# Kernel tuning notes

Measured on AMD Instinct MI355X. Metric: run time of the kernel, lower is better.

## Reference

```python
import jax, jax.numpy as jnp
import numpy as np
import math

SIZE = 64
NLAND = 8
N_ITER = 6


def setup_inputs() -> dict:
    key = jax.random.key(0)
    k1, k2, k3 = jax.random.split(key, 3)
    B, T, C = 4, 4096, 1024
    return {
        "q": jax.random.normal(k1, (B, T, C), dtype=jnp.float32),
        "k": jax.random.normal(k2, (B, T, C), dtype=jnp.float32),
        "v": jax.random.normal(k3, (B, T, C), dtype=jnp.float32),
    }


def _iterative_pinv(mat, n_iter=N_ITER):
    # Newton-Schulz iteration for pseudo-inverse of [..., m, m] kernel.
    m = mat.shape[-1]
    I = jnp.eye(m, dtype=mat.dtype)
    K = mat
    # NOTE: torch.max over the whole tensor (global scalar), faithful to source.
    V = (1.0 / jnp.max(jnp.sum(K, axis=-2))) * jnp.swapaxes(K, -1, -2)
    for _ in range(n_iter):
        KV = jnp.matmul(K, V)
        V = jnp.matmul(0.25 * V, 13.0 * I - jnp.matmul(KV, 15.0 * I - jnp.matmul(KV, 7.0 * I - KV)))
    return V


def reference(q, k, v):
    B, T, C = q.shape
    H = C // SIZE
    scale = 1.0 / math.sqrt(SIZE)
    # Faithful reshape (not transpose) as in the source module.
    qh = q.reshape(B, H, T, SIZE)
    kh = k.reshape(B, H, T, SIZE)
    vh = v.reshape(B, H, T, SIZE)
    # T % NLAND == 0 branch: landmark = segment mean over T//NLAND tokens.
    q_l = qh.reshape(B, H, NLAND, T // NLAND, SIZE).mean(axis=-2)  # [B,H,m,d]
    k_l = kh.reshape(B, H, NLAND, T // NLAND, SIZE).mean(axis=-2)
    kernel_1 = jax.nn.softmax(jnp.einsum('bhtd,bhmd->bhtm', qh, k_l) * scale, axis=-1)  # [B,H,T,m]
    kernel_2 = jax.nn.softmax(jnp.einsum('bhmd,bhnd->bhmn', q_l, k_l) * scale, axis=-1)  # [B,H,m,m]
    kernel_3 = jax.nn.softmax(jnp.einsum('bhmd,bhtd->bhmt', q_l, kh) * scale, axis=-1)  # [B,H,m,T]
    pinv = _iterative_pinv(kernel_2)  # [B,H,m,m]
    k3v = jnp.matmul(kernel_3, vh)    # [B,H,m,d]
    out = jnp.matmul(jnp.matmul(kernel_1, pinv), k3v)  # [B,H,T,d]
    return out.reshape(B, T, C)
```

## Files before the change

kernel.cpp:

```cpp
#include <hip/hip_runtime.h>
#include <math.h>

#define T_TOK 4096
#define DD 64
#define NHEADS 64
#define SEG 512
#define SCALE 0.125f

#define QL_OFF   0
#define KL_OFF   32768
#define K2_OFF   65536
#define CS_OFF   69632
#define KP_OFF   70144
#define PA_OFF   332288
#define PD_OFF   2429440
#define W2_OFF   2462208
#define LPQ_OFF  2494976

#define WAVE_BAR() __builtin_amdgcn_wave_barrier()

__global__ __launch_bounds__(256) void qsum_kernel(
    const float* __restrict__ q, float* __restrict__ ws) {
  int tid = threadIdx.x;
  const float4* q4 = (const float4*)q + (size_t)blockIdx.x * 2048;
  float4 x[8];
#pragma unroll
  for (int i = 0; i < 8; ++i) x[i] = q4[i * 256 + tid];
  float4 a = make_float4(0.f, 0.f, 0.f, 0.f);
#pragma unroll
  for (int i = 0; i < 8; ++i) {
    a.x += x[i].x; a.y += x[i].y; a.z += x[i].z; a.w += x[i].w;
  }
  __shared__ float4 red[16][17];
  red[tid >> 4][tid & 15] = a;
  __syncthreads();
  if (tid < 16) {
    float4 s = make_float4(0.f, 0.f, 0.f, 0.f);
#pragma unroll
    for (int g = 0; g < 16; ++g) {
      float4 r = red[g][tid];
      s.x += r.x; s.y += r.y; s.z += r.z; s.w += r.w;
    }
    ((float4*)(ws + LPQ_OFF))[blockIdx.x * 16 + tid] = s;
  }
}

__global__ __launch_bounds__(512) void prepq_kernel(float* __restrict__ ws) {
  int hb = blockIdx.x, tid = threadIdx.x;
  int m = tid >> 6, d = tid & 63;
  float s = 0.f;
#pragma unroll
  for (int c2 = 0; c2 < 4; ++c2)
    s += ws[LPQ_OFF + (size_t)(hb * 32 + m * 4 + c2) * 64 + d];
  ws[QL_OFF + hb * 512 + tid] = s * (1.f / (float)SEG);
}

#define STAGE_AND_CONSUME(K0,K1,K2,K3,V0,V1,V2,V3)                            \
  {                                                                           \
    int r0_ = lane >> 4, c0_ = (lane & 15) * 4;                               \
    *(float4*)&kt[r0_][c0_] = K0;       *(float4*)&vt[r0_][c0_] = V0;         \
    *(float4*)&kt[r0_+4][c0_] = K1;     *(float4*)&vt[r0_+4][c0_] = V1;       \
    *(float4*)&kt[r0_+8][c0_] = K2;     *(float4*)&vt[r0_+8][c0_] = V2;       \
    *(float4*)&kt[r0_+12][c0_] = K3;    *(float4*)&vt[r0_+12][c0_] = V3;      \
    ks.x += K0.x+K1.x+K2.x+K3.x; ks.y += K0.y+K1.y+K2.y+K3.y;                 \
    ks.z += K0.z+K1.z+K2.z+K3.z; ks.w += K0.w+K1.w+K2.w+K3.w;                 \
  }                                                                           \
  WAVE_BAR();                                                                 \
  _Pragma("unroll")                                                           \
  for (int rep_ = 0; rep_ < 2; ++rep_) {                                      \
    int t_ = rep_ * 8 + (lane >> 3);                                          \
    const float4* kr_ = (const float4*)&kt[t_][0];                            \
    const float4* qr_ = (const float4*)&qls[m][0];                            \
    float dp_ = 0.f;                                                          \
    _Pragma("unroll")                                                         \
    for (int d4_ = 0; d4_ < 16; ++d4_) {                                      \
      float4 kv_ = kr_[d4_], qv_ = qr_[d4_];                                  \
      dp_ += kv_.x*qv_.x + kv_.y*qv_.y + kv_.z*qv_.z + kv_.w*qv_.w;           \
    }                                                                         \
    float p_ = __expf(dp_ * SCALE);                                           \
    pl[t_][m] = p_;                                                           \
    den += p_;                                                                \
  }                                                                           \
  WAVE_BAR();                                                                 \
  _Pragma("unroll")                                                           \
  for (int t_ = 0; t_ < 16; ++t_) {                                           \
    float4 vv_ = *(const float4*)&vt[t_][d4i * 4];                            \
    float pa_ = pl[t_][g];                                                    \
    float pb_ = pl[t_][g + 4];                                                \
    acc0.x += pa_*vv_.x; acc0.y += pa_*vv_.y; acc0.z += pa_*vv_.z; acc0.w += pa_*vv_.w; \
    acc1.x += pb_*vv_.x; acc1.y += pb_*vv_.y; acc1.z += pb_*vv_.z; acc1.w += pb_*vv_.w; \
  }                                                                           \
  WAVE_BAR();

__global__ __launch_bounds__(256) void kvpass_kernel(
    const float* __restrict__ k, const float* __restrict__ v,
    float* __restrict__ ws) {
  int tid = threadIdx.x;
  int w = tid >> 6, lane = tid & 63;
  int gw = blockIdx.x * 4 + w;
  int hb = gw >> 6;
  __shared__ float qls[8][68];
  __shared__ float kt_all[4][16][68];
  __shared__ float vt_all[4][16][68];
  __shared__ float pl_all[4][16][9];
  float (*kt)[68] = kt_all[w];
  float (*vt)[68] = vt_all[w];
  float (*pl)[9]  = pl_all[w];

  if (tid < 128) {
    float4 x = ((const float4*)(ws + QL_OFF))[hb * 128 + tid];
    *(float4*)&qls[tid >> 4][(tid & 15) * 4] = x;
  }
  __syncthreads();

  int m = lane & 7, g = lane >> 4, d4i = lane & 15;
  size_t tokbase = (size_t)gw * 64;
  const float4* k4 = (const float4*)k + tokbase * 16;
  const float4* v4 = (const float4*)v + tokbase * 16;

  float4 ks = make_float4(0.f, 0.f, 0.f, 0.f);
  float den = 0.f;
  float4 acc0 = make_float4(0.f, 0.f, 0.f, 0.f);
  float4 acc1 = make_float4(0.f, 0.f, 0.f, 0.f);

  float4 ka0 = k4[lane],       ka1 = k4[64 + lane],
         ka2 = k4[128 + lane], ka3 = k4[192 + lane];
  float4 va0 = v4[lane],       va1 = v4[64 + lane],
         va2 = v4[128 + lane], va3 = v4[192 + lane];

#pragma unroll 1
  for (int t2 = 0; t2 < 2; ++t2) {
    int bB = (t2 * 2 + 1) * 256;
    float4 kb0 = k4[bB + lane],       kb1 = k4[bB + 64 + lane],
           kb2 = k4[bB + 128 + lane], kb3 = k4[bB + 192 + lane];
    float4 vb0 = v4[bB + lane],       vb1 = v4[bB + 64 + lane],
           vb2 = v4[bB + 128 + lane], vb3 = v4[bB + 192 + lane];

    STAGE_AND_CONSUME(ka0, ka1, ka2, ka3, va0, va1, va2, va3)

    if (t2 == 0) {
      ka0 = k4[512 + lane];       ka1 = k4[512 + 64 + lane];
      ka2 = k4[512 + 128 + lane]; ka3 = k4[512 + 192 + lane];
      va0 = v4[512 + lane];       va1 = v4[512 + 64 + lane];
      va2 = v4[512 + 128 + lane]; va3 = v4[512 + 192 + lane];
    }

    STAGE_AND_CONSUME(kb0, kb1, kb2, kb3, vb0, vb1, vb2, vb3)
  }
  ks.x += __shfl_xor(ks.x, 16, 64); ks.y += __shfl_xor(ks.y, 16, 64);
  ks.z += __shfl_xor(ks.z, 16, 64); ks.w += __shfl_xor(ks.w, 16, 64);
  ks.x += __shfl_xor(ks.x, 32, 64); ks.y += __shfl_xor(ks.y, 32, 64);
  ks.z += __shfl_xor(ks.z, 32, 64); ks.w += __shfl_xor(ks.w, 32, 64);
  if (lane < 16)
    ((float4*)(ws + KP_OFF))[gw * 16 + lane] = ks;
  den += __shfl_xor(den, 8, 64);
  den += __shfl_xor(den, 16, 64);
  den += __shfl_xor(den, 32, 64);
  if (lane < 8)
    ws[PD_OFF + (size_t)gw * 8 + lane] = den;
  ((float4*)(ws + PA_OFF))[((size_t)gw * 8 + g) * 16 + d4i] = acc0;
  ((float4*)(ws + PA_OFF))[((size_t)gw * 8 + g + 4) * 16 + d4i] = acc1;
}

__global__ __launch_bounds__(512) void prepk_kernel(float* __restrict__ ws) {
  int hb = blockIdx.x, tid = threadIdx.x;
  __shared__ float qls[8][68];
  __shared__ float kls[8][68];
  __shared__ float ee[8][9];
  int m = tid >> 6, d = tid & 63;
  float s = 0.f;
#pragma unroll
  for (int j = 0; j < 8; ++j)
    s += ws[KP_OFF + (size_t)(hb * 64 + m * 8 + j) * 64 + d];
  s *= (1.f / (float)SEG);
  kls[m][d] = s;
  ws[KL_OFF + hb * 512 + tid] = s;
  qls[m][d] = ws[QL_OFF + hb * 512 + tid];
  __syncthreads();
  if (tid < 64) {
    int i = tid >> 3, j = tid & 7;
    float dot = 0.f;
#pragma unroll
    for (int dd = 0; dd < 64; ++dd) dot += qls[i][dd] * kls[j][dd];
    ee[i][j] = __expf(dot * SCALE);
  }
  __syncthreads();
  if (tid < 64) {
    int i = tid >> 3, j = tid & 7;
    float ssum = 0.f;
#pragma unroll
    for (int jj = 0; jj < 8; ++jj) ssum += ee[i][jj];
    ws[K2_OFF + hb * 64 + tid] = ee[i][j] / ssum;
  }
  if (tid < 8) {
    float cs = 0.f;
    for (int ii = 0; ii < 8; ++ii) {
      float ssum = 0.f;
#pragma unroll
      for (int jj = 0; jj < 8; ++jj) ssum += ee[ii][jj];
      cs += ee[ii][tid] / ssum;
    }
    ws[CS_OFF + hb * 8 + tid] = cs;
  }
}

__global__ __launch_bounds__(512) void pinvw2_kernel(float* __restrict__ ws) {
  int hb = blockIdx.x, tid = threadIdx.x;
  __shared__ float k3vs[8][68];
  __shared__ float K[8][9], V[8][9], X[8][9], Y[8][9];
  __shared__ float smax;
  int m = tid >> 6, d = tid & 63;
  float s = 0.f, den = 0.f;
  for (int c = 0; c < 64; ++c) {
    s += ws[PA_OFF + (((size_t)hb * 64 + c) * 8 + m) * 64 + d];
    den += ws[PD_OFF + ((size_t)hb * 64 + c) * 8 + m];
  }
  k3vs[m][d] = s / den;
  if (tid < 64) {
    float mx = 0.f;
    for (int t = 0; t < 8; ++t) mx = fmaxf(mx, ws[CS_OFF + t * 64 + tid]);
    for (int off = 32; off; off >>= 1) mx = fmaxf(mx, __shfl_xor(mx, off, 64));
    if (tid == 0) smax = mx;
  }
  int i = (tid >> 3) & 7, j = tid & 7;
  if (tid < 64) K[i][j] = ws[K2_OFF + hb * 64 + tid];
  __syncthreads();
  if (tid < 64) V[i][j] = K[j][i] * (1.f / smax);
  __syncthreads();
  for (int it = 0; it < 6; ++it) {
    float x = 0.f;
    if (tid < 64) {
      for (int kk = 0; kk < 8; ++kk) x += K[i][kk] * V[kk][j];
      X[i][j] = x;
    }
    __syncthreads();
    float bm = 0.f;
    if (tid < 64) {
      for (int kk = 0; kk < 8; ++kk) bm += X[i][kk] * X[kk][j];
      bm = 7.f * x - bm;
      Y[i][j] = bm;
    }
    __syncthreads();
    float dm = 0.f;
    if (tid < 64) {
      for (int kk = 0; kk < 8; ++kk) dm += X[i][kk] * Y[kk][j];
      dm = 15.f * x - dm;
    }
    __syncthreads();
    if (tid < 64) Y[i][j] = dm;
    __syncthreads();
    float vd = 0.f;
    if (tid < 64) {
      for (int kk = 0; kk < 8; ++kk) vd += V[i][kk] * Y[kk][j];
      vd = 0.25f * (13.f * V[i][j] - vd);
    }
    __syncthreads();
    if (tid < 64) V[i][j] = vd;
    __syncthreads();
  }
  float o = 0.f;
#pragma unroll
  for (int jj = 0; jj < 8; ++jj) o += V[m][jj] * k3vs[jj][d];
  ws[W2_OFF + hb * 512 + tid] = o;
}

__global__ __launch_bounds__(256) void out_kernel(
    const float* __restrict__ q, float* __restrict__ out,
    const float* __restrict__ ws) {
  int tid = threadIdx.x;
  int w = tid >> 6, lane = tid & 63;
  int gw = blockIdx.x * 4 + w;
  int hb = gw >> 6;
  __shared__ float qt_all[4][16][68];
  __shared__ float pl_all[4][16][9];
  __shared__ float w2_all[4][8][68];
  float (*qt)[68] = qt_all[w];
  float (*pl)[9]  = pl_all[w];
  float (*w2)[68] = w2_all[w];

  int m = lane & 7;
  float4 klrow[16];
#pragma unroll
  for (int d4 = 0; d4 < 16; ++d4)
    klrow[d4] = ((const float4*)(ws + KL_OFF))[hb * 128 + m * 16 + d4];
#pragma unroll
  for (int i = 0; i < 2; ++i) {
    int f4 = i * 64 + lane;
    float4 y = ((const float4*)(ws + W2_OFF))[hb * 128 + f4];
    *(float4*)&w2[f4 >> 4][(f4 & 15) * 4] = y;
  }

  size_t base4 = (size_t)gw * 1024;
  const float4* q4 = (const float4*)q + base4;
  float4* o4 = (float4*)out + base4;
  float4 buf[2][4];
#pragma unroll
  for (int i = 0; i < 4; ++i) buf[0][i] = q4[i * 64 + lane];

#pragma unroll
  for (int tile = 0; tile < 4; ++tile) {
    int cur = tile & 1;
    if (tile < 3) {
#pragma unroll
      for (int i = 0; i < 4; ++i)
        buf[cur ^ 1][i] = q4[(tile + 1) * 256 + i * 64 + lane];
    }
#pragma unroll
    for (int i = 0; i < 4; ++i) {
      int f4 = i * 64 + lane;
      *(float4*)&qt[f4 >> 4][(f4 & 15) * 4] = buf[cur][i];
    }
    WAVE_BAR();
#pragma unroll
    for (int rep = 0; rep < 2; ++rep) {
      int t = rep * 8 + (lane >> 3);
      const float4* qr = (const float4*)&qt[t][0];
      float dot = 0.f;
#pragma unroll
      for (int d4 = 0; d4 < 16; ++d4) {
        float4 a = qr[d4];
        dot += a.x * klrow[d4].x + a.y * klrow[d4].y +
               a.z * klrow[d4].z + a.w * klrow[d4].w;
      }
      pl[t][m] = __expf(dot * SCALE);
    }
    WAVE_BAR();
#pragma unroll
    for (int i = 0; i < 4; ++i) {
      int t = i * 4 + (lane >> 4);
      int qd = lane & 15;
      float p0 = pl[t][0], p1 = pl[t][1], p2 = pl[t][2], p3 = pl[t][3];
      float p4 = pl[t][4], p5 = pl[t][5], p6 = pl[t][6], p7 = pl[t][7];
      float inv = 1.f / (p0 + p1 + p2 + p3 + p4 + p5 + p6 + p7);
      float4 acc = make_float4(0.f, 0.f, 0.f, 0.f);
      float pm[8] = {p0, p1, p2, p3, p4, p5, p6, p7};
#pragma unroll
      for (int m2 = 0; m2 < 8; ++m2) {
        float wgt = pm[m2] * inv;
        float4 wv = *(const float4*)&w2[m2][qd * 4];
        acc.x += wgt * wv.x; acc.y += wgt * wv.y;
        acc.z += wgt * wv.z; acc.w += wgt * wv.w;
      }
      o4[tile * 256 + i * 64 + lane] = acc;
    }
    WAVE_BAR();
  }
}

extern "C" void kernel_launch(void* const* d_in, const int* in_sizes, int n_in,
                              void* d_out, int out_size, void* d_ws, size_t ws_size,
                              hipStream_t stream) {
  const float* q = (const float*)d_in[0];
  const float* k = (const float*)d_in[1];
  const float* v = (const float*)d_in[2];
  float* out = (float*)d_out;
  float* ws = (float*)d_ws;

  qsum_kernel<<<2048, 256, 0, stream>>>(q, ws);
  prepq_kernel<<<NHEADS, 512, 0, stream>>>(ws);
  kvpass_kernel<<<1024, 256, 0, stream>>>(k, v, ws);
  prepk_kernel<<<NHEADS, 512, 0, stream>>>(ws);
  pinvw2_kernel<<<NHEADS, 512, 0, stream>>>(ws);
  out_kernel<<<1024, 256, 0, stream>>>(q, out, ws);
}
```

Measured before the change: 87.02 us.

## Replace LDS staging with register-resident DPP row reductions in kvpass and out kernels

```diff
diff --git a/kernel.cpp b/kernel.cpp
--- a/kernel.cpp
+++ b/kernel.cpp
@@ -17,7 +17,12 @@
 #define W2_OFF   2462208
 #define LPQ_OFF  2494976
 
-#define WAVE_BAR() __builtin_amdgcn_wave_barrier()
+#define ROR_ADD(x, imm)                                                        \
+  {                                                                            \
+    int t_ = __builtin_amdgcn_update_dpp(0, __float_as_int(x), 0x120 | (imm),  \
+                                         0xF, 0xF, false);                     \
+    x += __int_as_float(t_);                                                   \
+  }
 
 __global__ __launch_bounds__(256) void qsum_kernel(
     const float* __restrict__ q, float* __restrict__ ws) {
@@ -55,111 +60,91 @@
   ws[QL_OFF + hb * 512 + tid] = s * (1.f / (float)SEG);
 }
 
-#define STAGE_AND_CONSUME(K0,K1,K2,K3,V0,V1,V2,V3)                            \
-  {                                                                           \
-    int r0_ = lane >> 4, c0_ = (lane & 15) * 4;                               \
-    *(float4*)&kt[r0_][c0_] = K0;       *(float4*)&vt[r0_][c0_] = V0;         \
-    *(float4*)&kt[r0_+4][c0_] = K1;     *(float4*)&vt[r0_+4][c0_] = V1;       \
-    *(float4*)&kt[r0_+8][c0_] = K2;     *(float4*)&vt[r0_+8][c0_] = V2;       \
-    *(float4*)&kt[r0_+12][c0_] = K3;    *(float4*)&vt[r0_+12][c0_] = V3;      \
-    ks.x += K0.x+K1.x+K2.x+K3.x; ks.y += K0.y+K1.y+K2.y+K3.y;                 \
-    ks.z += K0.z+K1.z+K2.z+K3.z; ks.w += K0.w+K1.w+K2.w+K3.w;                 \
-  }                                                                           \
-  WAVE_BAR();                                                                 \
-  _Pragma("unroll")                                                           \
-  for (int rep_ = 0; rep_ < 2; ++rep_) {                                      \
-    int t_ = rep_ * 8 + (lane >> 3);                                          \
-    const float4* kr_ = (const float4*)&kt[t_][0];                            \
-    const float4* qr_ = (const float4*)&qls[m][0];                            \
-    float dp_ = 0.f;                                                          \
-    _Pragma("unroll")                                                         \
-    for (int d4_ = 0; d4_ < 16; ++d4_) {                                      \
-      float4 kv_ = kr_[d4_], qv_ = qr_[d4_];                                  \
-      dp_ += kv_.x*qv_.x + kv_.y*qv_.y + kv_.z*qv_.z + kv_.w*qv_.w;           \
-    }                                                                         \
-    float p_ = __expf(dp_ * SCALE);                                           \
-    pl[t_][m] = p_;                                                           \
-    den += p_;                                                                \
-  }                                                                           \
-  WAVE_BAR();                                                                 \
-  _Pragma("unroll")                                                           \
-  for (int t_ = 0; t_ < 16; ++t_) {                                           \
-    float4 vv_ = *(const float4*)&vt[t_][d4i * 4];                            \
-    float pa_ = pl[t_][g];                                                    \
-    float pb_ = pl[t_][g + 4];                                                \
-    acc0.x += pa_*vv_.x; acc0.y += pa_*vv_.y; acc0.z += pa_*vv_.z; acc0.w += pa_*vv_.w; \
-    acc1.x += pb_*vv_.x; acc1.y += pb_*vv_.y; acc1.z += pb_*vv_.z; acc1.w += pb_*vv_.w; \
-  }                                                                           \
-  WAVE_BAR();
-
-__global__ __launch_bounds__(256) void kvpass_kernel(
+#define KV_PROC(KK, VV)                                                        \
+  {                                                                            \
+    ks.x += KK.x; ks.y += KK.y; ks.z += KK.z; ks.w += KK.w;                    \
+    float dp[8];                                                               \
+    _Pragma("unroll")                                                          \
+    for (int j = 0; j < 8; ++j)                                                \
+      dp[j] = KK.x * ql[j].x + KK.y * ql[j].y + KK.z * ql[j].z +               \
+              KK.w * ql[j].w;                                                  \
+    _Pragma("unroll") for (int j = 0; j < 8; ++j) { ROR_ADD(dp[j], 8) }        \
+    _Pragma("unroll") for (int j = 0; j < 8; ++j) { ROR_ADD(dp[j], 4) }        \
+    _Pragma("unroll") for (int j = 0; j < 8; ++j) { ROR_ADD(dp[j], 2) }        \
+    _Pragma("unroll") for (int j = 0; j < 8; ++j) { ROR_ADD(dp[j], 1) }        \
+    _Pragma("unroll")                                                          \
+    for (int j = 0; j < 8; ++j) {                                              \
+      float p_ = __expf(dp[j] * SCALE);                                        \
+      den[j] += p_;                                                            \
+      acc[j].x += p_ * VV.x; acc[j].y += p_ * VV.y;                            \
+      acc[j].z += p_ * VV.z; acc[j].w += p_ * VV.w;                            \
+    }                                                                          \
+  }
+
+__global__ __launch_bounds__(256, 4) void kvpass_kernel(
     const float* __restrict__ k, const float* __restrict__ v,
     float* __restrict__ ws) {
   int tid = threadIdx.x;
   int w = tid >> 6, lane = tid & 63;
   int gw = blockIdx.x * 4 + w;
   int hb = gw >> 6;
-  __shared__ float qls[8][68];
-  __shared__ float kt_all[4][16][68];
-  __shared__ float vt_all[4][16][68];
-  __shared__ float pl_all[4][16][9];
-  float (*kt)[68] = kt_all[w];
-  float (*vt)[68] = vt_all[w];
-  float (*pl)[9]  = pl_all[w];
-
-  if (tid < 128) {
-    float4 x = ((const float4*)(ws + QL_OFF))[hb * 128 + tid];
-    *(float4*)&qls[tid >> 4][(tid & 15) * 4] = x;
-  }
-  __syncthreads();
-
-  int m = lane & 7, g = lane >> 4, d4i = lane & 15;
-  size_t tokbase = (size_t)gw * 64;
-  const float4* k4 = (const float4*)k + tokbase * 16;
-  const float4* v4 = (const float4*)v + tokbase * 16;
-
+  int d16 = lane & 15;
+
+  float4 ql[8];
+#pragma unroll
+  for (int j = 0; j < 8; ++j)
+    ql[j] = ((const float4*)(ws + QL_OFF))[hb * 128 + j * 16 + d16];
+
+  size_t base4 = (size_t)gw * 1024;
+  const float4* k4 = (const float4*)k + base4;
+  const float4* v4 = (const float4*)v + base4;
+
+  float4 acc[8];
+  float den[8];
+#pragma unroll
+  for (int j = 0; j < 8; ++j) {
+    acc[j] = make_float4(0.f, 0.f, 0.f, 0.f);
+    den[j] = 0.f;
+  }
   float4 ks = make_float4(0.f, 0.f, 0.f, 0.f);
-  float den = 0.f;
-  float4 acc0 = make_float4(0.f, 0.f, 0.f, 0.f);
-  float4 acc1 = make_float4(0.f, 0.f, 0.f, 0.f);
-
-  float4 ka0 = k4[lane],       ka1 = k4[64 + lane],
-         ka2 = k4[128 + lane], ka3 = k4[192 + lane];
-  float4 va0 = v4[lane],       va1 = v4[64 + lane],
-         va2 = v4[128 + lane], va3 = v4[192 + lane];
-
-#pragma unroll 1
-  for (int t2 = 0; t2 < 2; ++t2) {
-    int bB = (t2 * 2 + 1) * 256;
-    float4 kb0 = k4[bB + lane],       kb1 = k4[bB + 64 + lane],
-           kb2 = k4[bB + 128 + lane], kb3 = k4[bB + 192 + lane];
-    float4 vb0 = v4[bB + lane],       vb1 = v4[bB + 64 + lane],
-           vb2 = v4[bB + 128 + lane], vb3 = v4[bB + 192 + lane];
-
-    STAGE_AND_CONSUME(ka0, ka1, ka2, ka3, va0, va1, va2, va3)
-
-    if (t2 == 0) {
-      ka0 = k4[512 + lane];       ka1 = k4[512 + 64 + lane];
-      ka2 = k4[512 + 128 + lane]; ka3 = k4[512 + 192 + lane];
-      va0 = v4[512 + lane];       va1 = v4[512 + 64 + lane];
-      va2 = v4[512 + 128 + lane]; va3 = v4[512 + 192 + lane];
-    }
-
-    STAGE_AND_CONSUME(kb0, kb1, kb2, kb3, vb0, vb1, vb2, vb3)
+
+#pragma unroll 2
+  for (int it = 0; it < 16; ++it) {
+    float4 kk = k4[it * 64 + lane];
+    float4 vv = v4[it * 64 + lane];
+    KV_PROC(kk, vv)
+  }
+
+#pragma unroll
+  for (int j = 0; j < 8; ++j) {
+    acc[j].x += __shfl_xor(acc[j].x, 16, 64);
+    acc[j].y += __shfl_xor(acc[j].y, 16, 64);
+    acc[j].z += __shfl_xor(acc[j].z, 16, 64);
+    acc[j].w += __shfl_xor(acc[j].w, 16, 64);
+    acc[j].x += __shfl_xor(acc[j].x, 32, 64);
+    acc[j].y += __shfl_xor(acc[j].y, 32, 64);
+    acc[j].z += __shfl_xor(acc[j].z, 32, 64);
+    acc[j].w += __shfl_xor(acc[j].w, 32, 64);
+    den[j] += __shfl_xor(den[j], 16, 64);
+    den[j] += __shfl_xor(den[j], 32, 64);
   }
   ks.x += __shfl_xor(ks.x, 16, 64); ks.y += __shfl_xor(ks.y, 16, 64);
   ks.z += __shfl_xor(ks.z, 16, 64); ks.w += __shfl_xor(ks.w, 16, 64);
   ks.x += __shfl_xor(ks.x, 32, 64); ks.y += __shfl_xor(ks.y, 32, 64);
   ks.z += __shfl_xor(ks.z, 32, 64); ks.w += __shfl_xor(ks.w, 32, 64);
-  if (lane < 16)
+
+  if (lane < 16) {
+#pragma unroll
+    for (int j = 0; j < 8; ++j)
+      ((float4*)(ws + PA_OFF))[((size_t)gw * 8 + j) * 16 + lane] = acc[j];
     ((float4*)(ws + KP_OFF))[gw * 16 + lane] = ks;
-  den += __shfl_xor(den, 8, 64);
-  den += __shfl_xor(den, 16, 64);
-  den += __shfl_xor(den, 32, 64);
-  if (lane < 8)
-    ws[PD_OFF + (size_t)gw * 8 + lane] = den;
-  ((float4*)(ws + PA_OFF))[((size_t)gw * 8 + g) * 16 + d4i] = acc0;
-  ((float4*)(ws + PA_OFF))[((size_t)gw * 8 + g + 4) * 16 + d4i] = acc1;
+  }
+  if (lane == 0) {
+    *(float4*)&ws[PD_OFF + (size_t)gw * 8] =
+        make_float4(den[0], den[1], den[2], den[3]);
+    *(float4*)&ws[PD_OFF + (size_t)gw * 8 + 4] =
+        make_float4(den[4], den[5], den[6], den[7]);
+  }
 }
 
 __global__ __launch_bounds__(512) void prepk_kernel(float* __restrict__ ws) {
@@ -264,86 +249,56 @@
   ws[W2_OFF + hb * 512 + tid] = o;
 }
 
-__global__ __launch_bounds__(256) void out_kernel(
+#define OUT_PROC(QQ, IDX)                                                      \
+  {                                                                            \
+    float dp[8];                                                               \
+    _Pragma("unroll")                                                          \
+    for (int j = 0; j < 8; ++j)                                                \
+      dp[j] = QQ.x * kl[j].x + QQ.y * kl[j].y + QQ.z * kl[j].z +               \
+              QQ.w * kl[j].w;                                                  \
+    _Pragma("unroll") for (int j = 0; j < 8; ++j) { ROR_ADD(dp[j], 8) }        \
+    _Pragma("unroll") for (int j = 0; j < 8; ++j) { ROR_ADD(dp[j], 4) }        \
+    _Pragma("unroll") for (int j = 0; j < 8; ++j) { ROR_ADD(dp[j], 2) }        \
+    _Pragma("unroll") for (int j = 0; j < 8; ++j) { ROR_ADD(dp[j], 1) }        \
+    float p_[8];                                                               \
+    float s_ = 0.f;                                                            \
+    _Pragma("unroll")                                                          \
+    for (int j = 0; j < 8; ++j) { p_[j] = __expf(dp[j] * SCALE); s_ += p_[j]; }\
+    float inv_ = 1.f / s_;                                                     \
+    float4 o_ = make_float4(0.f, 0.f, 0.f, 0.f);                               \
+    _Pragma("unroll")                                                          \
+    for (int j = 0; j < 8; ++j) {                                              \
+      float wg_ = p_[j] * inv_;                                                \
+      o_.x += wg_ * w2r[j].x; o_.y += wg_ * w2r[j].y;                          \
+      o_.z += wg_ * w2r[j].z; o_.w += wg_ * w2r[j].w;                          \
+    }                                                                          \
+    o4[IDX] = o_;                                                              \
+  }
+
+__global__ __launch_bounds__(256, 4) void out_kernel(
     const float* __restrict__ q, float* __restrict__ out,
     const float* __restrict__ ws) {
   int tid = threadIdx.x;
   int w = tid >> 6, lane = tid & 63;
   int gw = blockIdx.x * 4 + w;
   int hb = gw >> 6;
-  __shared__ float qt_all[4][16][68];
-  __shared__ float pl_all[4][16][9];
-  __shared__ float w2_all[4][8][68];
-  float (*qt)[68] = qt_all[w];
-  float (*pl)[9]  = pl_all[w];
-  float (*w2)[68] = w2_all[w];
-
-  int m = lane & 7;
-  float4 klrow[16];
-#pragma unroll
-  for (int d4 = 0; d4 < 16; ++d4)
-    klrow[d4] = ((const float4*)(ws + KL_OFF))[hb * 128 + m * 16 + d4];
-#pragma unroll
-  for (int i = 0; i < 2; ++i) {
-    int f4 = i * 64 + lane;
-    float4 y = ((const float4*)(ws + W2_OFF))[hb * 128 + f4];
-    *(float4*)&w2[f4 >> 4][(f4 & 15) * 4] = y;
+  int d16 = lane & 15;
+
+  float4 kl[8], w2r[8];
+#pragma unroll
+  for (int j = 0; j < 8; ++j) {
+    kl[j]  = ((const float4*)(ws + KL_OFF))[hb * 128 + j * 16 + d16];
+    w2r[j] = ((const float4*)(ws + W2_OFF))[hb * 128 + j * 16 + d16];
   }
 
   size_t base4 = (size_t)gw * 1024;
   const float4* q4 = (const float4*)q + base4;
   float4* o4 = (float4*)out + base4;
-  float4 buf[2][4];
-#pragma unroll
-  for (int i = 0; i < 4; ++i) buf[0][i] = q4[i * 64 + lane];
-
-#pragma unroll
-  for (int tile = 0; tile < 4; ++tile) {
-    int cur = tile & 1;
-    if (tile < 3) {
-#pragma unroll
-      for (int i = 0; i < 4; ++i)
-        buf[cur ^ 1][i] = q4[(tile + 1) * 256 + i * 64 + lane];
-    }
-#pragma unroll
-    for (int i = 0; i < 4; ++i) {
-      int f4 = i * 64 + lane;
-      *(float4*)&qt[f4 >> 4][(f4 & 15) * 4] = buf[cur][i];
-    }
-    WAVE_BAR();
-#pragma unroll
-    for (int rep = 0; rep < 2; ++rep) {
-      int t = rep * 8 + (lane >> 3);
-      const float4* qr = (const float4*)&qt[t][0];
-      float dot = 0.f;
-#pragma unroll
-      for (int d4 = 0; d4 < 16; ++d4) {
-        float4 a = qr[d4];
-        dot += a.x * klrow[d4].x + a.y * klrow[d4].y +
-               a.z * klrow[d4].z + a.w * klrow[d4].w;
-      }
-      pl[t][m] = __expf(dot * SCALE);
-    }
-    WAVE_BAR();
-#pragma unroll
-    for (int i = 0; i < 4; ++i) {
-      int t = i * 4 + (lane >> 4);
-      int qd = lane & 15;
-      float p0 = pl[t][0], p1 = pl[t][1], p2 = pl[t][2], p3 = pl[t][3];
-      float p4 = pl[t][4], p5 = pl[t][5], p6 = pl[t][6], p7 = pl[t][7];
-      float inv = 1.f / (p0 + p1 + p2 + p3 + p4 + p5 + p6 + p7);
-      float4 acc = make_float4(0.f, 0.f, 0.f, 0.f);
-      float pm[8] = {p0, p1, p2, p3, p4, p5, p6, p7};
-#pragma unroll
-      for (int m2 = 0; m2 < 8; ++m2) {
-        float wgt = pm[m2] * inv;
-        float4 wv = *(const float4*)&w2[m2][qd * 4];
-        acc.x += wgt * wv.x; acc.y += wgt * wv.y;
-        acc.z += wgt * wv.z; acc.w += wgt * wv.w;
-      }
-      o4[tile * 256 + i * 64 + lane] = acc;
-    }
-    WAVE_BAR();
+
+#pragma unroll 2
+  for (int it = 0; it < 16; ++it) {
+    float4 qq = q4[it * 64 + lane];
+    OUT_PROC(qq, it * 64 + lane)
   }
 }
 
```

Result: no change. 85.57 us (-1.7%).
